# Kernel optimization log

Measured on AMD Instinct MI355X. Metric: run time of the kernel, lower is better.

Reference implementation:

```python
import jax, jax.numpy as jnp
import numpy as np

EMBED = 256
HEADS = 8
LEVELS = 4
POINTS = 4
HEAD_DIM = EMBED // HEADS
SHAPES = [(100, 100), (50, 50), (25, 25), (13, 13)]  # (H, W) per level
NUM_KEYS = sum(h * w for h, w in SHAPES)  # 13294
LEVEL_STARTS = np.cumsum([0] + [h * w for h, w in SHAPES])[:-1]
B, Q = 8, 900


def _offset_bias():
    # Faithful reproduction of the torch _reset_parameters sampling_offsets bias.
    th = np.arange(HEADS, dtype=np.float32) * (2.0 * np.pi / HEADS)
    g = np.stack([np.cos(th), np.sin(th)], -1)
    g = g / np.abs(g).max(-1, keepdims=True)
    g = np.tile(g[:, None, None, :], (1, LEVELS, POINTS, 1))
    g = g * np.arange(1, POINTS + 1, dtype=np.float32)[None, None, :, None]
    return jnp.asarray(g.reshape(-1), dtype=jnp.float32)


def setup_inputs() -> dict:
    key = jax.random.key(0)
    ks = jax.random.split(key, 12)
    s = 1.0 / np.sqrt(EMBED)
    return {
        "query": jax.random.normal(ks[0], (B, Q, EMBED), jnp.float32),
        "reference_points": jax.random.uniform(ks[1], (B, Q, LEVELS, 2), jnp.float32),
        "value": jax.random.normal(ks[2], (B, NUM_KEYS, EMBED), jnp.float32),
        "spatial_shapes": jnp.asarray(np.array(SHAPES, dtype=np.int32)),
        "level_start_index": jnp.asarray(LEVEL_STARTS.astype(np.int32)),
        "W_off": jax.random.normal(ks[3], (EMBED, HEADS * LEVELS * POINTS * 2), jnp.float32) * 0.01,
        "b_off": _offset_bias(),
        "W_attn": jax.random.normal(ks[4], (EMBED, HEADS * LEVELS * POINTS), jnp.float32) * 0.01,
        "b_attn": jnp.zeros((HEADS * LEVELS * POINTS,), jnp.float32),
        "W_val": jax.random.normal(ks[5], (EMBED, EMBED), jnp.float32) * s,
        "b_val": jnp.zeros((EMBED,), jnp.float32),
        "W_out": jax.random.normal(ks[6], (EMBED, EMBED), jnp.float32) * s,
        "b_out": jnp.zeros((EMBED,), jnp.float32),
    }


def _bilinear(vflat, x, y, H, W):
    # vflat: [BH, H*W, D]; x, y: [BH, Q, P] in unnormalized pixel coords.
    # grid_sample(mode='bilinear', padding_mode='zeros', align_corners=False)
    BH, Qn, Pn = x.shape
    D = vflat.shape[-1]
    x0f = jnp.floor(x); y0f = jnp.floor(y)
    wx = x - x0f; wy = y - y0f
    x0 = x0f.astype(jnp.int32); y0 = y0f.astype(jnp.int32)

    def gather(xi, yi):
        inb = (xi >= 0) & (xi < W) & (yi >= 0) & (yi < H)
        idx = jnp.clip(yi, 0, H - 1) * W + jnp.clip(xi, 0, W - 1)
        g = jnp.take_along_axis(vflat, idx.reshape(BH, Qn * Pn, 1), axis=1)
        return g.reshape(BH, Qn, Pn, D) * inb[..., None].astype(vflat.dtype)

    v00 = gather(x0, y0)
    v01 = gather(x0 + 1, y0)
    v10 = gather(x0, y0 + 1)
    v11 = gather(x0 + 1, y0 + 1)
    return (v00 * ((1 - wx) * (1 - wy))[..., None]
            + v01 * (wx * (1 - wy))[..., None]
            + v10 * ((1 - wx) * wy)[..., None]
            + v11 * (wx * wy)[..., None])


def _msda(value_hd, shapes_np, starts_np, loc, attw):
    # value_hd: [B, K, H, D]; loc: [B, Q, H, L, P, 2]; attw: [B, Q, H, L, P]
    Bn, K, Hn, D = value_hd.shape
    Qn, Pn = loc.shape[1], loc.shape[4]
    out = jnp.zeros((Bn * Hn, Qn, D), value_hd.dtype)
    for l, (Hl, Wl) in enumerate(shapes_np):
        s = int(starts_np[l])
        v = value_hd[:, s:s + Hl * Wl]                      # [B, Hl*Wl, H, D]
        v = v.reshape(Bn, Hl * Wl, Hn, D).transpose(0, 2, 1, 3)
        vflat = v.reshape(Bn * Hn, Hl * Wl, D)
        # sampling_grid = 2*loc - 1; grid_sample align_corners=False -> x = loc*W - 0.5
        lx = loc[:, :, :, l, :, 0].transpose(0, 2, 1, 3).reshape(Bn * Hn, Qn, Pn)
        ly = loc[:, :, :, l, :, 1].transpose(0, 2, 1, 3).reshape(Bn * Hn, Qn, Pn)
        samp = _bilinear(vflat, lx * Wl - 0.5, ly * Hl - 0.5, Hl, Wl)  # [BH,Q,P,D]
        w = attw[:, :, :, l, :].transpose(0, 2, 1, 3).reshape(Bn * Hn, Qn, Pn)
        out = out + jnp.einsum('bqpd,bqp->bqd', samp, w)
    return out.reshape(Bn, Hn, Qn, D).transpose(0, 2, 1, 3).reshape(Bn, Qn, Hn * D)


def reference(query, reference_points, value, spatial_shapes, level_start_index,
              W_off, b_off, W_attn, b_attn, W_val, b_val, W_out, b_out):
    shapes_np = np.asarray(spatial_shapes)
    starts_np = np.asarray(level_start_index)
    Bn, Qn, _ = query.shape
    K = value.shape[1]

    v = value @ W_val + b_val                              # [B, K, E]
    v = v.reshape(Bn, K, HEADS, HEAD_DIM)

    off = (query @ W_off + b_off).reshape(Bn, Qn, HEADS, LEVELS, POINTS, 2)
    aw = (query @ W_attn + b_attn).reshape(Bn, Qn, HEADS, LEVELS * POINTS)
    aw = jax.nn.softmax(aw, axis=-1).reshape(Bn, Qn, HEADS, LEVELS, POINTS)

    # offset_normalizer = (W, H) per level
    norm = jnp.asarray(shapes_np[:, ::-1].astype(np.float32)).reshape(1, 1, 1, LEVELS, 1, 2)
    loc = reference_points[:, :, None, :, None, :] + off / norm  # [B,Q,H,L,P,2]

    out = _msda(v, shapes_np, starts_np, loc, aw)          # [B, Q, E]
    return out @ W_out + b_out
```

## Files before the change

kernel.cpp:

```cpp
#include <hip/hip_runtime.h>
#include <hip/hip_bf16.h>
#include <math.h>
#include <type_traits>

#define BATCH 8
#define QLEN 900
#define HEADS 8
#define LEVELS 4
#define POINTS 4
#define NUM_KEYS 13294
#define BQ (BATCH * QLEN)
#define MROWS_V (BATCH * NUM_KEYS)
#define VTILES (MROWS_V / 16)
#define VBLOCKS 512
#define TPB 13

__constant__ const int c_LH[4] = {100, 50, 25, 13};
__constant__ const int c_LW[4] = {100, 50, 25, 13};
__constant__ const int c_LS[4] = {0, 10000, 12500, 13125};

typedef __attribute__((ext_vector_type(8))) short bfrag;
typedef __attribute__((ext_vector_type(4))) float ffrag;

static __device__ __forceinline__ unsigned short f2bf(float f) {
    __hip_bfloat16 h = __float2bfloat16(f);
    return *(unsigned short*)&h;
}
static __device__ __forceinline__ float bf2f(unsigned int u16) {
    unsigned int v = u16 << 16;
    float f;
    __builtin_memcpy(&f, &v, 4);
    return f;
}
static __device__ __forceinline__ unsigned long long pack4bf(float4 v) {
    return (unsigned long long)f2bf(v.x)
         | ((unsigned long long)f2bf(v.y) << 16)
         | ((unsigned long long)f2bf(v.z) << 32)
         | ((unsigned long long)f2bf(v.w) << 48);
}

__global__ __launch_bounds__(256)
void prep_kernel(const float* __restrict__ W_val, const float* __restrict__ W_off,
                 const float* __restrict__ W_attn, const float* __restrict__ W_out,
                 const float* __restrict__ b_off, const float* __restrict__ b_attn,
                 unsigned short* __restrict__ Wv, unsigned short* __restrict__ Woa,
                 unsigned short* __restrict__ Wo, float* __restrict__ boa) {
    const int id = blockIdx.x * 256 + threadIdx.x;
    if (id < 65536) {
        const int n = id >> 8, k = id & 255;
        Wv[id] = f2bf(W_val[k * 256 + n]);
    } else if (id < 131072) {
        const int t = id - 65536;
        const int n = t >> 8, k = t & 255;
        Woa[t] = f2bf(W_off[k * 256 + n]);
    } else if (id < 163840) {
        const int t = id - 131072;
        const int n = t >> 8, k = t & 255;
        Woa[65536 + t] = f2bf(W_attn[k * 128 + n]);
    } else if (id < 229376) {
        const int t = id - 163840;
        const int n = t >> 8, k = t & 255;
        Wo[t] = f2bf(W_out[k * 256 + n]);
    } else if (id < 229760) {
        const int t = id - 229376;
        boa[t] = (t < 256) ? b_off[t] : b_attn[t - 256];
    }
}

#define VSTEP(T, LREG)                                                        \
  do {                                                                        \
    const char* abuf = (const char*)&Abuf[0][0] + rb * 8192;                  \
    ffrag acc[2];                                                             \
    _Pragma("unroll")                                                         \
    for (int j_ = 0; j_ < 2; ++j_) acc[j_] = (ffrag){0.f, 0.f, 0.f, 0.f};     \
    _Pragma("unroll")                                                         \
    for (int ks_ = 0; ks_ < 8; ++ks_) {                                       \
      const int ub_ = (ks_ * 64 + quad * 16) ^ ((ln & 7) << 4);               \
      const bfrag af_ = *(const bfrag*)(abuf + ln * 512 + ub_);               \
      _Pragma("unroll")                                                       \
      for (int j_ = 0; j_ < 2; ++j_)                                          \
        acc[j_] = __builtin_amdgcn_mfma_f32_16x16x32_bf16(af_, b[j_][ks_],    \
                                                          acc[j_], 0, 0, 0); \
    }                                                                         \
    if ((T) + 1 < t1) {                                                       \
      const int wb_ = (rb + 1 == 3) ? 0 : rb + 1;                             \
      char* dbuf_ = (char*)&Abuf[0][0] + wb_ * 8192;                          \
      _Pragma("unroll")                                                       \
      for (int i_ = 0; i_ < 2; ++i_)                                          \
        *(unsigned long long*)(dbuf_ + dsoff[i_]) = pack4bf(LREG[i_]);        \
      if ((T) + 3 < t1) {                                                     \
        const float4* ap_ = Af4 + (size_t)((T) + 3) * 1024 + tid;             \
        _Pragma("unroll")                                                     \
        for (int i_ = 0; i_ < 2; ++i_) LREG[i_] = ap_[i_ * 512];              \
      }                                                                       \
    }                                                                         \
    const int rowb_ = (T) * 16 + quad * 4;                                    \
    _Pragma("unroll")                                                         \
    for (int r_ = 0; r_ < 4; ++r_) {                                          \
      const unsigned row_ = rowb_ + r_;                                       \
      const unsigned bb_ = row_ / NUM_KEYS;                                   \
      const unsigned key_ = row_ - bb_ * NUM_KEYS;                            \
      _Pragma("unroll")                                                       \
      for (int j_ = 0; j_ < 2; ++j_) {                                        \
        const int col_ = n0 + j_ * 16 + ln;                                   \
        const int h_ = col_ >> 5, d_ = col_ & 31;                             \
        C[((size_t)(bb_ * 8 + h_) * NUM_KEYS + key_) * 32 + d_] =             \
            f2bf(acc[j_][r_] + bj[j_]);                                       \
      }                                                                       \
    }                                                                         \
    asm volatile("s_waitcnt lgkmcnt(0)" ::: "memory");                        \
    __builtin_amdgcn_s_barrier();                                             \
    rb = (rb + 1 == 3) ? 0 : rb + 1;                                          \
  } while (0)

__global__ __launch_bounds__(512, 4)
void gemm_val_stream(const float* __restrict__ A, const unsigned short* __restrict__ WT,
                     const float* __restrict__ bias, unsigned short* __restrict__ C) {
    __shared__ __align__(16) unsigned short Abuf[3][16 * 256];
    const int tid = threadIdx.x;
    const int wave = tid >> 6;
    const int lane = tid & 63;
    const int ln = lane & 15;
    const int quad = lane >> 4;
    const int n0 = wave * 32;

    bfrag b[2][8];
#pragma unroll
    for (int j = 0; j < 2; ++j) {
        const unsigned short* bp = WT + (size_t)(n0 + j * 16 + ln) * 256 + quad * 8;
#pragma unroll
        for (int ks = 0; ks < 8; ++ks) b[j][ks] = *(const bfrag*)(bp + ks * 32);
    }
    float bj[2];
#pragma unroll
    for (int j = 0; j < 2; ++j) bj[j] = bias[n0 + j * 16 + ln];

    const int t0 = blockIdx.x * TPB;
    const int t1 = min(t0 + TPB, VTILES);
    if (t0 >= t1) return;

    int dsoff[2];
#pragma unroll
    for (int i = 0; i < 2; ++i) {
        const int f = i * 512 + tid;
        const int r = f >> 6;
        const int cb = (f & 63) * 8;
        dsoff[i] = r * 512 + (cb ^ ((r & 7) << 4));
    }

    const float4* Af4 = (const float4*)A;

    float4 L0[2], L1[2];
    {
        const float4* ap = Af4 + (size_t)t0 * 1024 + tid;
        float4 P[2];
#pragma unroll
        for (int i = 0; i < 2; ++i) P[i] = ap[i * 512];
#pragma unroll
        for (int i = 0; i < 2; ++i)
            *(unsigned long long*)((char*)&Abuf[0][0] + dsoff[i]) = pack4bf(P[i]);
    }
    if (t0 + 1 < t1) {
        const float4* ap = Af4 + (size_t)(t0 + 1) * 1024 + tid;
#pragma unroll
        for (int i = 0; i < 2; ++i) L0[i] = ap[i * 512];
    }
    if (t0 + 2 < t1) {
        const float4* ap = Af4 + (size_t)(t0 + 2) * 1024 + tid;
#pragma unroll
        for (int i = 0; i < 2; ++i) L1[i] = ap[i * 512];
    }
    asm volatile("s_waitcnt lgkmcnt(0)" ::: "memory");
    __builtin_amdgcn_s_barrier();

    int rb = 0;
    int t = t0;
    while (t + 1 < t1) {
        VSTEP(t, L0);
        VSTEP(t + 1, L1);
        t += 2;
    }
    if (t < t1) VSTEP(t, L0);
}

#define GST 72

template <typename AT, typename CT>
__global__ __launch_bounds__(256)
void gemm_mfma(const AT* __restrict__ A, const unsigned short* __restrict__ WT,
               const float* __restrict__ bias, CT* __restrict__ C,
               int M, int ldc) {
    __shared__ unsigned short As[64 * GST];
    __shared__ unsigned short Bs[128 * GST];
    const int tid = threadIdx.x;
    const int wave = tid >> 6;
    const int lane = tid & 63;
    const int ln = lane & 15;
    const int quad = lane >> 4;
    const int m0 = blockIdx.x * 64;
    const int n0 = blockIdx.y * 128;

    ffrag acc[8];
#pragma unroll
    for (int j = 0; j < 8; ++j) acc[j] = (ffrag){0.f, 0.f, 0.f, 0.f};

    const int ar = tid >> 2;
    const int akc = (tid & 3) * 16;
    const int brow = tid >> 1;
    const int bkc = (tid & 1) * 32;
    const bool a_ok = (m0 + ar) < M;
    const AT* a_src = A + (size_t)(m0 + ar) * 256 + akc;
    const unsigned short* b_src = WT + (size_t)(n0 + brow) * 256 + bkc;

    for (int k0 = 0; k0 < 256; k0 += 64) {
        unsigned short* adst = &As[ar * GST + akc];
        if constexpr (std::is_same<AT, float>::value) {
            float4 f0, f1, f2, f3;
            if (a_ok) {
                const float4* p = (const float4*)(a_src + k0);
                f0 = p[0]; f1 = p[1]; f2 = p[2]; f3 = p[3];
            } else {
                f0 = make_float4(0.f, 0.f, 0.f, 0.f);
                f1 = f0; f2 = f0; f3 = f0;
            }
            float v[16] = {f0.x, f0.y, f0.z, f0.w, f1.x, f1.y, f1.z, f1.w,
                           f2.x, f2.y, f2.z, f2.w, f3.x, f3.y, f3.z, f3.w};
            unsigned short u[16];
#pragma unroll
            for (int i = 0; i < 16; ++i) u[i] = f2bf(v[i]);
            ((uint4*)adst)[0] = ((uint4*)u)[0];
            ((uint4*)adst)[1] = ((uint4*)u)[1];
        } else {
            uint4 u0, u1;
            if (a_ok) {
                const uint4* p = (const uint4*)(a_src + k0);
                u0 = p[0]; u1 = p[1];
            } else {
                u0 = make_uint4(0, 0, 0, 0);
                u1 = u0;
            }
            ((uint4*)adst)[0] = u0;
            ((uint4*)adst)[1] = u1;
        }
        {
            const uint4* src = (const uint4*)(b_src + k0);
            uint4* dst = (uint4*)&Bs[brow * GST + bkc];
#pragma unroll
            for (int i = 0; i < 4; ++i) dst[i] = src[i];
        }
        __syncthreads();

#pragma unroll
        for (int ks = 0; ks < 2; ++ks) {
            const int koff = ks * 32 + quad * 8;
            bfrag af = *(const bfrag*)&As[(wave * 16 + ln) * GST + koff];
#pragma unroll
            for (int j = 0; j < 8; ++j) {
                bfrag bf = *(const bfrag*)&Bs[(j * 16 + ln) * GST + koff];
                acc[j] = __builtin_amdgcn_mfma_f32_16x16x32_bf16(af, bf, acc[j], 0, 0, 0);
            }
        }
        __syncthreads();
    }

#pragma unroll
    for (int j = 0; j < 8; ++j) {
        const int col = n0 + j * 16 + ln;
        const float bb = bias[col];
#pragma unroll
        for (int r = 0; r < 4; ++r) {
            const int row = m0 + wave * 16 + quad * 4 + r;
            if (row < M) {
                const float v = acc[j][r] + bb;
                if constexpr (std::is_same<CT, unsigned short>::value) {
                    C[(size_t)row * ldc + col] = f2bf(v);
                } else {
                    C[(size_t)row * ldc + col] = v;
                }
            }
        }
    }
}

__global__ __launch_bounds__(256, 4)
void msda_sample_kernel(const float* __restrict__ offattn,
                        const float* __restrict__ rp,
                        const unsigned short* __restrict__ vb,
                        unsigned short* __restrict__ outb) {
    const int bq0 = blockIdx.x * 8;
    const int tid = threadIdx.x;

    __shared__ float s_w[8][128];
    __shared__ float s_x[8][128];
    __shared__ float s_y[8][128];

#pragma unroll
    for (int i = 0; i < 4; ++i) {
        const int e = i * 256 + tid;
        const int q = e >> 7, t = e & 127;
        s_w[q][t] = offattn[(size_t)(bq0 + q) * 384 + 256 + t];
    }
    __syncthreads();

    if (tid < 64) {
        const int q = tid >> 3, h = tid & 7;
        float m = -1e30f;
#pragma unroll
        for (int i = 0; i < 16; ++i) m = fmaxf(m, s_w[q][h * 16 + i]);
        float e[16];
        float s = 0.f;
#pragma unroll
        for (int i = 0; i < 16; ++i) {
            e[i] = expf(s_w[q][h * 16 + i] - m);
            s += e[i];
        }
        const float inv = 1.f / s;
#pragma unroll
        for (int i = 0; i < 16; ++i) s_w[q][h * 16 + i] = e[i] * inv;
    }

#pragma unroll
    for (int i = 0; i < 4; ++i) {
        const int e = i * 256 + tid;
        const int q = e >> 7, t = e & 127;
        const int h = t >> 4, l = (t >> 2) & 3, p = t & 3;
        const int bq = bq0 + q;
        const float2 off = *(const float2*)(offattn + (size_t)bq * 384 + h * 32 + l * 8 + p * 2);
        const float Wl = (float)c_LW[l];
        const float Hl = (float)c_LH[l];
        const float rx = rp[((size_t)bq * 4 + l) * 2 + 0];
        const float ry = rp[((size_t)bq * 4 + l) * 2 + 1];
        s_x[q][t] = (rx + off.x / Wl) * Wl - 0.5f;
        s_y[q][t] = (ry + off.y / Hl) * Hl - 0.5f;
    }
    __syncthreads();

    const int q = tid >> 5;
    const int s = tid & 31;
    const int h = s >> 2;
    const int dp = s & 3;
    const int bq = bq0 + q;
    const int b = bq / QLEN;
    const unsigned short* vbase = vb + (size_t)(b * 8 + h) * NUM_KEYS * 32 + dp * 8;

    float acc[8];
#pragma unroll
    for (int d = 0; d < 8; ++d) acc[d] = 0.f;

#pragma unroll
    for (int l = 0; l < LEVELS; ++l) {
        const int Hl = c_LH[l];
        const int Wl = c_LW[l];
        const int s0 = c_LS[l];
#pragma unroll 2
        for (int p = 0; p < POINTS; ++p) {
            const int t2 = h * 16 + l * 4 + p;
            const float x = s_x[q][t2];
            const float y = s_y[q][t2];
            const float w = s_w[q][t2];
            const float x0f = floorf(x);
            const float y0f = floorf(y);
            const float wx = x - x0f;
            const float wy = y - y0f;
            const int x0 = (int)x0f;
            const int y0 = (int)y0f;
            const float mx0 = ((unsigned)x0 < (unsigned)Wl) ? 1.f : 0.f;
            const float mx1 = ((unsigned)(x0 + 1) < (unsigned)Wl) ? 1.f : 0.f;
            const float my0 = ((unsigned)y0 < (unsigned)Hl) ? 1.f : 0.f;
            const float my1 = ((unsigned)(y0 + 1) < (unsigned)Hl) ? 1.f : 0.f;
            const int xc0 = min(max(x0, 0), Wl - 1);
            const int xc1 = min(max(x0 + 1, 0), Wl - 1);
            const int yc0 = min(max(y0, 0), Hl - 1);
            const int yc1 = min(max(y0 + 1, 0), Hl - 1);
            const float a00 = w * (1.f - wx) * (1.f - wy) * mx0 * my0;
            const float a01 = w * wx * (1.f - wy) * mx1 * my0;
            const float a10 = w * (1.f - wx) * wy * mx0 * my1;
            const float a11 = w * wx * wy * mx1 * my1;
            const size_t k00 = (size_t)(s0 + yc0 * Wl + xc0) * 32;
            const size_t k01 = (size_t)(s0 + yc0 * Wl + xc1) * 32;
            const size_t k10 = (size_t)(s0 + yc1 * Wl + xc0) * 32;
            const size_t k11 = (size_t)(s0 + yc1 * Wl + xc1) * 32;
            const uint4 r00 = *(const uint4*)(vbase + k00);
            const uint4 r01 = *(const uint4*)(vbase + k01);
            const uint4 r10 = *(const uint4*)(vbase + k10);
            const uint4 r11 = *(const uint4*)(vbase + k11);
            const unsigned int w00[4] = {r00.x, r00.y, r00.z, r00.w};
            const unsigned int w01[4] = {r01.x, r01.y, r01.z, r01.w};
            const unsigned int w10[4] = {r10.x, r10.y, r10.z, r10.w};
            const unsigned int w11[4] = {r11.x, r11.y, r11.z, r11.w};
#pragma unroll
            for (int i = 0; i < 4; ++i) {
                const float v00l = bf2f(w00[i] & 0xffffu), v00h = bf2f(w00[i] >> 16);
                const float v01l = bf2f(w01[i] & 0xffffu), v01h = bf2f(w01[i] >> 16);
                const float v10l = bf2f(w10[i] & 0xffffu), v10h = bf2f(w10[i] >> 16);
                const float v11l = bf2f(w11[i] & 0xffffu), v11h = bf2f(w11[i] >> 16);
                acc[i * 2 + 0] = fmaf(a00, v00l, fmaf(a01, v01l, fmaf(a10, v10l, fmaf(a11, v11l, acc[i * 2 + 0]))));
                acc[i * 2 + 1] = fmaf(a00, v00h, fmaf(a01, v01h, fmaf(a10, v10h, fmaf(a11, v11h, acc[i * 2 + 1]))));
            }
        }
    }

    unsigned short o[8];
#pragma unroll
    for (int d = 0; d < 8; ++d) o[d] = f2bf(acc[d]);
    *(uint4*)(outb + (size_t)bq * 256 + h * 32 + dp * 8) = *(uint4*)o;
}

extern "C" void kernel_launch(void* const* d_in, const int* in_sizes, int n_in,
                              void* d_out, int out_size, void* d_ws, size_t ws_size,
                              hipStream_t stream) {
    const float* query  = (const float*)d_in[0];
    const float* rp     = (const float*)d_in[1];
    const float* value  = (const float*)d_in[2];
    const float* W_off  = (const float*)d_in[5];
    const float* b_off  = (const float*)d_in[6];
    const float* W_attn = (const float*)d_in[7];
    const float* b_attn = (const float*)d_in[8];
    const float* W_val  = (const float*)d_in[9];
    const float* b_val  = (const float*)d_in[10];
    const float* W_out  = (const float*)d_in[11];
    const float* b_out  = (const float*)d_in[12];
    float* out = (float*)d_out;

    char* w = (char*)d_ws;
    unsigned short* ws_vb = (unsigned short*)w;
    w += (size_t)MROWS_V * 256 * 2;
    float* ws_offattn = (float*)w;
    w += (size_t)BQ * 384 * 4;
    unsigned short* ws_msda = (unsigned short*)w;
    w += (size_t)BQ * 256 * 2;
    unsigned short* ws_Wv = (unsigned short*)w;  w += 256 * 256 * 2;
    unsigned short* ws_Woa = (unsigned short*)w; w += 384 * 256 * 2;
    unsigned short* ws_Wo = (unsigned short*)w;  w += 256 * 256 * 2;
    float* ws_boa = (float*)w;

    prep_kernel<<<898, 256, 0, stream>>>(W_val, W_off, W_attn, W_out,
                                         b_off, b_attn, ws_Wv, ws_Woa, ws_Wo, ws_boa);

    gemm_val_stream<<<VBLOCKS, 512, 0, stream>>>(value, ws_Wv, b_val, ws_vb);

    {
        dim3 grid((BQ + 63) / 64, 3);
        gemm_mfma<float, float><<<grid, 256, 0, stream>>>(
            query, ws_Woa, ws_boa, ws_offattn, BQ, 384);
    }
    msda_sample_kernel<<<BQ / 8, 256, 0, stream>>>(ws_offattn, rp, ws_vb, ws_msda);

    {
        dim3 grid((BQ + 63) / 64, 2);
        gemm_mfma<unsigned short, float><<<grid, 256, 0, stream>>>(
            ws_msda, ws_Wo, b_out, out, BQ, 256);
    }
}
```

Baseline: 250.2 us.

## Fuse output projection GEMM into MSDA sampling kernel via LDS and MFMA

The sampling kernel now writes its bf16 result for 8 queries into a swizzled LDS tile and runs the output projection there with MFMA, adding the bias and storing float output directly. The separate output GEMM launch and the round-trip of the sampled intermediate through global memory go away. In exchange, a 16-row MFMA tile is only half filled (8 rows), every block re-reads the full Wo weight matrix from global/L2, and the extra LDS may reduce occupancy.

```diff
diff --git a/kernel.cpp b/kernel.cpp
--- a/kernel.cpp
+++ b/kernel.cpp
@@ -283,16 +283,19 @@
 }
 
 __global__ __launch_bounds__(256, 4)
-void msda_sample_kernel(const float* __restrict__ offattn,
-                        const float* __restrict__ rp,
-                        const unsigned short* __restrict__ vb,
-                        unsigned short* __restrict__ outb) {
+void msda_fused_kernel(const float* __restrict__ offattn,
+                       const float* __restrict__ rp,
+                       const unsigned short* __restrict__ vb,
+                       const unsigned short* __restrict__ Wo,
+                       const float* __restrict__ b_out,
+                       float* __restrict__ out) {
     const int bq0 = blockIdx.x * 8;
     const int tid = threadIdx.x;
 
     __shared__ float s_w[8][128];
     __shared__ float s_x[8][128];
     __shared__ float s_y[8][128];
+    __shared__ __align__(16) unsigned short s_o[16 * 256];
 
 #pragma unroll
     for (int i = 0; i < 4; ++i) {
@@ -339,8 +342,7 @@
     const int s = tid & 31;
     const int h = s >> 2;
     const int dp = s & 3;
-    const int bq = bq0 + q;
-    const int b = bq / QLEN;
+    const int b = (bq0 + q) / QLEN;
     const unsigned short* vbase = vb + (size_t)(b * 8 + h) * NUM_KEYS * 32 + dp * 8;
 
     float acc[8];
@@ -400,10 +402,46 @@
         }
     }
 
-    unsigned short o[8];
-#pragma unroll
-    for (int d = 0; d < 8; ++d) o[d] = f2bf(acc[d]);
-    *(uint4*)(outb + (size_t)bq * 256 + h * 32 + dp * 8) = *(uint4*)o;
+    {
+        unsigned short o[8];
+#pragma unroll
+        for (int d = 0; d < 8; ++d) o[d] = f2bf(acc[d]);
+        const int cb = (h * 32 + dp * 8) * 2;
+        *(uint4*)((char*)s_o + q * 512 + (cb ^ ((q & 7) << 4))) = *(uint4*)o;
+    }
+    __syncthreads();
+
+    {
+        const int wv = tid >> 6;
+        const int lane = tid & 63;
+        const int ln = lane & 15;
+        const int quad = lane >> 4;
+        const int n0 = wv * 64;
+
+        ffrag oacc[4];
+#pragma unroll
+        for (int j = 0; j < 4; ++j) oacc[j] = (ffrag){0.f, 0.f, 0.f, 0.f};
+#pragma unroll
+        for (int ks = 0; ks < 8; ++ks) {
+            const int cbk = (ks * 64 + quad * 16) ^ ((ln & 7) << 4);
+            const bfrag af = *(const bfrag*)((const char*)s_o + ln * 512 + cbk);
+#pragma unroll
+            for (int j = 0; j < 4; ++j) {
+                const bfrag bf = *(const bfrag*)(Wo + (size_t)(n0 + j * 16 + ln) * 256 + ks * 32 + quad * 8);
+                oacc[j] = __builtin_amdgcn_mfma_f32_16x16x32_bf16(af, bf, oacc[j], 0, 0, 0);
+            }
+        }
+        if (quad < 2) {
+#pragma unroll
+            for (int j = 0; j < 4; ++j) {
+                const int col = n0 + j * 16 + ln;
+                const float bb = b_out[col];
+#pragma unroll
+                for (int r = 0; r < 4; ++r)
+                    out[(size_t)(bq0 + quad * 4 + r) * 256 + col] = oacc[j][r] + bb;
+            }
+        }
+    }
 }
 
 extern "C" void kernel_launch(void* const* d_in, const int* in_sizes, int n_in,
@@ -433,6 +471,7 @@
     unsigned short* ws_Woa = (unsigned short*)w; w += 384 * 256 * 2;
     unsigned short* ws_Wo = (unsigned short*)w;  w += 256 * 256 * 2;
     float* ws_boa = (float*)w;
+    (void)ws_msda;
 
     prep_kernel<<<898, 256, 0, stream>>>(W_val, W_off, W_attn, W_out,
                                          b_off, b_attn, ws_Wv, ws_Woa, ws_Wo, ws_boa);
@@ -444,11 +483,6 @@
         gemm_mfma<float, float><<<grid, 256, 0, stream>>>(
             query, ws_Woa, ws_boa, ws_offattn, BQ, 384);
     }
-    msda_sample_kernel<<<BQ / 8, 256, 0, stream>>>(ws_offattn, rp, ws_vb, ws_msda);
-
-    {
-        dim3 grid((BQ + 63) / 64, 2);
-        gemm_mfma<unsigned short, float><<<grid, 256, 0, stream>>>(
-            ws_msda, ws_Wo, b_out, out, BQ, 256);
-    }
-}
+    msda_fused_kernel<<<BQ / 8, 256, 0, stream>>>(ws_offattn, rp, ws_vb,
+                                                  ws_Wo, b_out, out);
+}
```

Result: no change. 252.4 us (+0.9%).

## Split MSDA sampling blocks by head-half and remap blocks per XCD for L2 locality

Applied to the files above, without the earlier changes.

Each sampling block now handles 16 queries for 4 of the 8 heads instead of 8 queries for all heads. Block IDs are remapped so that each XCD gets a contiguous range of work, which puts one head-half's value data on the same L2 slices. The goal is better cache reuse of the bf16 value tensor during the bilinear gathers. The grid stays at 900 blocks. The mapping hardcodes 8 XCDs and the 113/112 split.

```diff
diff --git a/kernel.cpp b/kernel.cpp
--- a/kernel.cpp
+++ b/kernel.cpp
@@ -287,43 +287,51 @@
                         const float* __restrict__ rp,
                         const unsigned short* __restrict__ vb,
                         unsigned short* __restrict__ outb) {
-    const int bq0 = blockIdx.x * 8;
+    const int orig = blockIdx.x;
+    const int xcd = orig & 7;
+    const int idx = orig >> 3;
+    const int wgid = (xcd < 4) ? (xcd * 113 + idx) : (452 + (xcd - 4) * 112 + idx);
+    const int hh = wgid / 450;
+    const int pos = wgid - hh * 450;
+    const int bq0 = pos * 16;
+    const int hb = hh * 4;
     const int tid = threadIdx.x;
 
-    __shared__ float s_w[8][128];
-    __shared__ float s_x[8][128];
-    __shared__ float s_y[8][128];
+    __shared__ float s_w[16][64];
+    __shared__ float s_x[16][64];
+    __shared__ float s_y[16][64];
 
 #pragma unroll
     for (int i = 0; i < 4; ++i) {
         const int e = i * 256 + tid;
-        const int q = e >> 7, t = e & 127;
-        s_w[q][t] = offattn[(size_t)(bq0 + q) * 384 + 256 + t];
+        const int q = e >> 6, t = e & 63;
+        const int h = hb + (t >> 4), lp = t & 15;
+        s_w[q][t] = offattn[(size_t)(bq0 + q) * 384 + 256 + h * 16 + lp];
     }
     __syncthreads();
 
     if (tid < 64) {
-        const int q = tid >> 3, h = tid & 7;
+        const int q = tid >> 2, h4 = tid & 3;
         float m = -1e30f;
 #pragma unroll
-        for (int i = 0; i < 16; ++i) m = fmaxf(m, s_w[q][h * 16 + i]);
+        for (int i = 0; i < 16; ++i) m = fmaxf(m, s_w[q][h4 * 16 + i]);
         float e[16];
-        float s = 0.f;
+        float ssum = 0.f;
 #pragma unroll
         for (int i = 0; i < 16; ++i) {
-            e[i] = expf(s_w[q][h * 16 + i] - m);
-            s += e[i];
-        }
-        const float inv = 1.f / s;
-#pragma unroll
-        for (int i = 0; i < 16; ++i) s_w[q][h * 16 + i] = e[i] * inv;
+            e[i] = expf(s_w[q][h4 * 16 + i] - m);
+            ssum += e[i];
+        }
+        const float inv = 1.f / ssum;
+#pragma unroll
+        for (int i = 0; i < 16; ++i) s_w[q][h4 * 16 + i] = e[i] * inv;
     }
 
 #pragma unroll
     for (int i = 0; i < 4; ++i) {
         const int e = i * 256 + tid;
-        const int q = e >> 7, t = e & 127;
-        const int h = t >> 4, l = (t >> 2) & 3, p = t & 3;
+        const int q = e >> 6, t = e & 63;
+        const int h = hb + (t >> 4), l = (t >> 2) & 3, p = t & 3;
         const int bq = bq0 + q;
         const float2 off = *(const float2*)(offattn + (size_t)bq * 384 + h * 32 + l * 8 + p * 2);
         const float Wl = (float)c_LW[l];
@@ -335,12 +343,13 @@
     }
     __syncthreads();
 
-    const int q = tid >> 5;
-    const int s = tid & 31;
-    const int h = s >> 2;
+    const int q = tid >> 4;
+    const int s = tid & 15;
+    const int h4 = s >> 2;
     const int dp = s & 3;
     const int bq = bq0 + q;
     const int b = bq / QLEN;
+    const int h = hb + h4;
     const unsigned short* vbase = vb + (size_t)(b * 8 + h) * NUM_KEYS * 32 + dp * 8;
 
     float acc[8];
@@ -354,7 +363,7 @@
         const int s0 = c_LS[l];
 #pragma unroll 2
         for (int p = 0; p < POINTS; ++p) {
-            const int t2 = h * 16 + l * 4 + p;
+            const int t2 = h4 * 16 + l * 4 + p;
             const float x = s_x[q][t2];
             const float y = s_y[q][t2];
             const float w = s_w[q][t2];
@@ -444,7 +453,7 @@
         gemm_mfma<float, float><<<grid, 256, 0, stream>>>(
             query, ws_Woa, ws_boa, ws_offattn, BQ, 384);
     }
-    msda_sample_kernel<<<BQ / 8, 256, 0, stream>>>(ws_offattn, rp, ws_vb, ws_msda);
+    msda_sample_kernel<<<900, 256, 0, stream>>>(ws_offattn, rp, ws_vb, ws_msda);
 
     {
         dim3 grid((BQ + 63) / 64, 2);
```

Result: faster. 244.7 us (-2.2%).
